# Kernel tuning notes

Measured on AMD Instinct MI355X. Metric: run time of the kernel, lower is better.

Reference implementation:

```python
import jax, jax.numpy as jnp
import numpy as np

N_EXPERTS = 8
TOP_K = 2
D_MODEL = 1024
D_FF = 4 * D_MODEL

def setup_inputs() -> dict:
    key = jax.random.key(0)
    ks = jax.random.split(key, 5)
    s_in = 1.0 / np.sqrt(D_MODEL)
    s_ff = 1.0 / np.sqrt(D_FF)
    return {
        "x": jax.random.normal(ks[0], (2, 2048, D_MODEL), dtype=jnp.float32),
        "Wr": jax.random.normal(ks[1], (N_EXPERTS, D_MODEL), dtype=jnp.float32) * s_in,
        "W1": jax.random.normal(ks[2], (N_EXPERTS, D_FF, D_MODEL), dtype=jnp.float32) * s_in,
        "W2": jax.random.normal(ks[3], (N_EXPERTS, D_MODEL, D_FF), dtype=jnp.float32) * s_ff,
        "W3": jax.random.normal(ks[4], (N_EXPERTS, D_FF, D_MODEL), dtype=jnp.float32) * s_in,
    }

def reference(x, Wr, W1, W2, W3):
    B, S, D = x.shape
    T = B * S
    xf = x.reshape(T, D)
    logits = xf @ Wr.T                         # [T, E]
    probs = jax.nn.softmax(logits, axis=-1)
    top_p, top_i = jax.lax.top_k(probs, TOP_K)  # [T, K]
    top_p = top_p / jnp.sum(top_p, axis=-1, keepdims=True)
    # per-token combine weight for each expert: [T, E]
    onehot = jax.nn.one_hot(top_i, N_EXPERTS, dtype=x.dtype)  # [T, K, E]
    cw = jnp.einsum('tke,tk->te', onehot, top_p)
    out = jnp.zeros_like(xf)
    for e in range(N_EXPERTS):  # fixed small structural loop over experts
        h = jax.nn.silu(xf @ W1[e].T) * (xf @ W3[e].T)  # [T, F]
        y = h @ W2[e].T                                 # [T, D]
        out = out + cw[:, e:e+1] * y
    importance = jnp.sum(probs, axis=0)                 # [E]
    load = jnp.sum(jnp.sum(onehot, axis=1), axis=0)     # [E]
    aux_loss = jnp.sum(importance * load) * (N_EXPERTS / (T ** 2 + 1e-06))
    return out.reshape(B, S, D), aux_loss
```

## Files before the change

### kernel.cpp

```cpp
#include <hip/hip_runtime.h>

#define T_TOK 4096
#define DM 1024
#define DF 4096
#define NE 8
#define BM 256
#define RCAP 10240
#define MAXT 40
#define ACH_B 32768
#define CHUNK_B 8192

typedef _Float16 f16x8 __attribute__((ext_vector_type(8)));
typedef float f32x4 __attribute__((ext_vector_type(4)));

#define MFMA16(a, b, c) __builtin_amdgcn_mfma_f32_16x16x32_f16(a, b, c, 0, 0, 0)
#define RAW_BAR() __builtin_amdgcn_s_barrier()
#define VMCNT(n) asm volatile("s_waitcnt vmcnt(" #n ")" ::: "memory")

__device__ __forceinline__ ushort f2h_bits(float f) {
    _Float16 h = (_Float16)f;
    return __builtin_bit_cast(unsigned short, h);
}

__device__ __forceinline__ unsigned int pk2(float a, float b) {
    return __builtin_bit_cast(unsigned int, __builtin_amdgcn_cvt_pkrtz(a, b));
}

__device__ __forceinline__ uint4 pack8(float4 a, float4 b) {
    uint4 r;
    r.x = pk2(a.x, a.y); r.y = pk2(a.z, a.w);
    r.z = pk2(b.x, b.y); r.w = pk2(b.z, b.w);
    return r;
}

__device__ __forceinline__ void gll16(const void* g, void* l) {
    __builtin_amdgcn_global_load_lds(
        (const __attribute__((address_space(1))) unsigned int*)g,
        (__attribute__((address_space(3))) unsigned int*)l, 16, 0, 0);
}

__global__ __launch_bounds__(256) void k_init(float* __restrict__ out,
                                              int* __restrict__ misc,
                                              int* __restrict__ row_tok) {
    int i = blockIdx.x * 256 + threadIdx.x;
    if (i < T_TOK * DM + 1) out[i] = 0.f;
    if (i < RCAP) row_tok[i] = -1;
    if (i < 256) misc[i] = 0;
}

__global__ __launch_bounds__(64) void k_router(const float* __restrict__ x,
                                               const float* __restrict__ Wr,
                                               float* __restrict__ probs,
                                               int* __restrict__ topi,
                                               float* __restrict__ topw,
                                               int* __restrict__ cnt) {
    int t = blockIdx.x;
    int lane = threadIdx.x;
    const float* xr = x + (size_t)t * DM;
    float s[NE];
#pragma unroll
    for (int e = 0; e < NE; e++) s[e] = 0.f;
    for (int j = lane; j < DM; j += 64) {
        float xv = xr[j];
#pragma unroll
        for (int e = 0; e < NE; e++) s[e] += xv * Wr[e * DM + j];
    }
#pragma unroll
    for (int off = 32; off > 0; off >>= 1) {
#pragma unroll
        for (int e = 0; e < NE; e++) s[e] += __shfl_xor(s[e], off, 64);
    }
    if (lane == 0) {
        float mx = s[0];
#pragma unroll
        for (int e = 1; e < NE; e++) mx = fmaxf(mx, s[e]);
        float ex[NE], sum = 0.f;
#pragma unroll
        for (int e = 0; e < NE; e++) { ex[e] = expf(s[e] - mx); sum += ex[e]; }
        float inv = 1.f / sum;
        float p[NE];
#pragma unroll
        for (int e = 0; e < NE; e++) { p[e] = ex[e] * inv; probs[t * NE + e] = p[e]; }
        int i0 = 0;
#pragma unroll
        for (int e = 1; e < NE; e++) if (p[e] > p[i0]) i0 = e;
        int i1 = (i0 == 0) ? 1 : 0;
#pragma unroll
        for (int e = 0; e < NE; e++) if (e != i0 && p[e] > p[i1]) i1 = e;
        float w0 = p[i0], w1 = p[i1], winv = 1.f / (w0 + w1);
        topi[2 * t] = i0;     topw[2 * t] = w0 * winv;
        topi[2 * t + 1] = i1; topw[2 * t + 1] = w1 * winv;
        atomicAdd(&cnt[i0], 1);
        atomicAdd(&cnt[i1], 1);
    }
}

__global__ __launch_bounds__(256) void k_scan(const float* __restrict__ probs,
                                              const int* __restrict__ cnt,
                                              int* __restrict__ poff,
                                              int* __restrict__ texp,
                                              float* __restrict__ aux_out) {
    __shared__ float red[256 * NE];
    int tid = threadIdx.x;
    float part[NE];
#pragma unroll
    for (int e = 0; e < NE; e++) part[e] = 0.f;
    for (int t = tid; t < T_TOK; t += 256) {
#pragma unroll
        for (int e = 0; e < NE; e++) part[e] += probs[t * NE + e];
    }
#pragma unroll
    for (int e = 0; e < NE; e++) red[tid * NE + e] = part[e];
    __syncthreads();
    for (int s2 = 128; s2 > 0; s2 >>= 1) {
        if (tid < s2) {
#pragma unroll
            for (int e = 0; e < NE; e++) red[tid * NE + e] += red[(tid + s2) * NE + e];
        }
        __syncthreads();
    }
    if (tid == 0) {
        float al = 0.f;
#pragma unroll
        for (int e = 0; e < NE; e++) al += red[e] * (float)cnt[e];
        *aux_out = al * (8.0f / (16777216.0f + 1e-6f));
        int run = 0, tix = 0;
        for (int e = 0; e < NE; e++) {
            poff[e] = run;
            int nt = (cnt[e] + BM - 1) / BM;
            for (int i = 0; i < nt; i++) texp[tix++] = e;
            run += nt * BM;
        }
    }
}

__global__ __launch_bounds__(256) void k_assign(const int* __restrict__ topi,
                                                const float* __restrict__ topw,
                                                const int* __restrict__ poff,
                                                int* __restrict__ fill,
                                                int* __restrict__ row_tok,
                                                float* __restrict__ row_w) {
    int t = blockIdx.x * 256 + threadIdx.x;
    if (t >= T_TOK) return;
#pragma unroll
    for (int k = 0; k < 2; k++) {
        int e = topi[2 * t + k];
        int pos = atomicAdd(&fill[e], 1);
        int r = poff[e] + pos;
        row_tok[r] = t;
        row_w[r] = topw[2 * t + k];
    }
}

__global__ __launch_bounds__(256) void k_convert(const float* __restrict__ src,
                                                 ushort* __restrict__ dst,
                                                 int row_len) {
    int nk = row_len >> 6;
    int kt = blockIdx.x, rt = blockIdx.y;
    int tid = threadIdx.x;
    int r = tid >> 2, c0 = (tid & 3) * 16;
    const float* s = src + (size_t)(rt * 64 + r) * row_len + kt * 64 + c0;
    float4 v0 = *(const float4*)(s);
    float4 v1 = *(const float4*)(s + 4);
    float4 v2 = *(const float4*)(s + 8);
    float4 v3 = *(const float4*)(s + 12);
    char* chunk = (char*)dst + ((size_t)rt * nk + kt) * CHUNK_B;
    int sw = (r & 7) << 4;
    *(uint4*)(chunk + r * 128 + ((2 * c0) ^ sw)) = pack8(v0, v1);
    *(uint4*)(chunk + r * 128 + ((2 * c0 + 16) ^ sw)) = pack8(v2, v3);
}

__global__ __launch_bounds__(512) void k_gather_t(const float* __restrict__ x,
                                                  const int* __restrict__ row_tok,
                                                  ushort* __restrict__ xg) {
    int kt = blockIdx.x, rt = blockIdx.y;
    int tid = threadIdx.x;
    int r = tid >> 1, c0 = (tid & 1) * 32;
    int tok = row_tok[rt * BM + r];
    char* chunk = (char*)xg + ((size_t)rt * 16 + kt) * ACH_B;
    int sw = (r & 7) << 4;
    if (tok >= 0) {
        const float* s = x + (size_t)tok * DM + kt * 64 + c0;
#pragma unroll
        for (int j = 0; j < 4; j++) {
            float4 va = *(const float4*)(s + j * 8);
            float4 vb = *(const float4*)(s + j * 8 + 4);
            *(uint4*)(chunk + r * 128 + ((c0 * 2 + j * 16) ^ sw)) = pack8(va, vb);
        }
    } else {
        uint4 z = {0, 0, 0, 0};
#pragma unroll
        for (int j = 0; j < 4; j++)
            *(uint4*)(chunk + r * 128 + ((c0 * 2 + j * 16) ^ sw)) = z;
    }
}

__global__ __launch_bounds__(512, 2) void k_g1(const ushort* __restrict__ xg,
                                               const ushort* __restrict__ W1h,
                                               const ushort* __restrict__ W3h,
                                               const int* __restrict__ texp,
                                               ushort* __restrict__ hbuf) {
    __shared__ __align__(16) char lds[131072];
    int b = blockIdx.x;
    int sz = (b & 7) * 160 + (b >> 3);
    int ct = sz / MAXT, rt = sz % MAXT;
    int e = texp[rt];
    int tid = threadIdx.x, lane = tid & 63, wv = tid >> 6;
    int wr = wv >> 1, wc = wv & 1;

    const char* Ac  = (const char*)xg + (size_t)rt * 16 * ACH_B;
    const char* B1c = (const char*)W1h + ((size_t)(e * 64 + ct * 2) * 16) * CHUNK_B;
    const char* B3c = (const char*)W3h + ((size_t)(e * 64 + ct * 2) * 16) * CHUNK_B;

    const f32x4 fz = {0.f, 0.f, 0.f, 0.f};
    f32x4 acc1[4][4], acc3[4][4];
#pragma unroll
    for (int m = 0; m < 4; m++)
#pragma unroll
        for (int n = 0; n < 4; n++) { acc1[m][n] = fz; acc3[m][n] = fz; }

    f16x8 af[4], bf[4];
    int kb_base = (lane >> 4) * 16;

#define ST_A(kt_, b_, h_) {                                                        \
        const char* s_ = Ac + (kt_) * ACH_B + (h_) * 16384 + wv * 2048 + lane * 16; \
        char* d_ = lds + (b_) * 65536 + (h_) * 16384 + wv * 2048;                   \
        gll16(s_, d_); gll16(s_ + 1024, d_ + 1024); }
#define ST_B(Bc_, kt_, b_, off_) {                                                          \
        gll16(Bc_ + (kt_) * 8192 + wv * 1024 + lane * 16,                                    \
              lds + (b_) * 65536 + (off_) + wv * 1024);                                      \
        gll16(Bc_ + 131072 + (kt_) * 8192 + wv * 1024 + lane * 16,                           \
              lds + (b_) * 65536 + (off_) + 8192 + wv * 1024); }
#define DS_A(b_, ks_) _Pragma("unroll") for (int m = 0; m < 4; m++) {              \
        int r_ = wr * 64 + m * 16 + (lane & 15);                                   \
        af[m] = *(const f16x8*)(lds + (b_) * 65536 + r_ * 128 +                    \
                                 (((ks_) * 64 + kb_base) ^ ((r_ & 7) << 4))); }
#define DS_B(b_, off_, ks_) _Pragma("unroll") for (int n = 0; n < 4; n++) {        \
        int c_ = wc * 64 + n * 16 + (lane & 15);                                   \
        bf[n] = *(const f16x8*)(lds + (b_) * 65536 + (off_) + c_ * 128 +           \
                                 (((ks_) * 64 + kb_base) ^ ((c_ & 7) << 4))); }
#define MM(accX) _Pragma("unroll") for (int n = 0; n < 4; n++)                     \
        _Pragma("unroll") for (int m = 0; m < 4; m++)                              \
            accX[m][n] = MFMA16(af[m], bf[n], accX[m][n]);

    ST_A(0, 0, 0); ST_A(0, 0, 1); ST_B(B1c, 0, 0, 32768); ST_B(B3c, 0, 0, 49152);
    VMCNT(2);
    RAW_BAR();

    for (int it = 0; it < 8; ++it) {
        int t1 = 2 * it + 1;
        int t2 = 2 * it + 2;
        DS_A(0, 0); DS_B(0, 32768, 0);
        ST_A(t1, 1, 0);
        RAW_BAR();
        __builtin_amdgcn_s_setprio(1); MM(acc1); __builtin_amdgcn_s_setprio(0);
        VMCNT(2);
        RAW_BAR();
        DS_B(0, 49152, 0);
        ST_A(t1, 1, 1);
        RAW_BAR();
        __builtin_amdgcn_s_setprio(1); MM(acc3); __builtin_amdgcn_s_setprio(0);
        RAW_BAR();
        DS_A(0, 1); DS_B(0, 32768, 1);
        ST_B(B1c, t1, 1, 32768);
        RAW_BAR();
        __builtin_amdgcn_s_setprio(1); MM(acc1); __builtin_amdgcn_s_setprio(0);
        RAW_BAR();
        DS_B(0, 49152, 1);
        ST_B(B3c, t1, 1, 49152);
        RAW_BAR();
        __builtin_amdgcn_s_setprio(1); MM(acc3); __builtin_amdgcn_s_setprio(0);
        VMCNT(2);
        RAW_BAR();
        DS_A(1, 0); DS_B(1, 32768, 0);
        if (it < 7) ST_A(t2, 0, 0);
        RAW_BAR();
        __builtin_amdgcn_s_setprio(1); MM(acc1); __builtin_amdgcn_s_setprio(0);
        if (it < 7) { VMCNT(2); } else { VMCNT(0); }
        RAW_BAR();
        DS_B(1, 49152, 0);
        if (it < 7) ST_A(t2, 0, 1);
        RAW_BAR();
        __builtin_amdgcn_s_setprio(1); MM(acc3); __builtin_amdgcn_s_setprio(0);
        RAW_BAR();
        DS_A(1, 1); DS_B(1, 32768, 1);
        if (it < 7) ST_B(B1c, t2, 0, 32768);
        RAW_BAR();
        __builtin_amdgcn_s_setprio(1); MM(acc1); __builtin_amdgcn_s_setprio(0);
        RAW_BAR();
        DS_B(1, 49152, 1);
        if (it < 7) ST_B(B3c, t2, 0, 49152);
        RAW_BAR();
        __builtin_amdgcn_s_setprio(1); MM(acc3); __builtin_amdgcn_s_setprio(0);
        if (it < 7) { VMCNT(2); }
        RAW_BAR();
    }
#undef ST_A
#undef ST_B
#undef DS_A
#undef DS_B
#undef MM

#pragma unroll
    for (int m = 0; m < 4; m++) {
#pragma unroll
        for (int i = 0; i < 4; i++) {
            int rl = wr * 64 + m * 16 + (lane >> 4) * 4 + i;
            int sw = (rl & 7) << 4;
#pragma unroll
            for (int n = 0; n < 4; n++) {
                int fl = wc * 64 + n * 16 + (lane & 15);
                float a1 = acc1[m][n][i], a3 = acc3[m][n][i];
                float h = (a1 / (1.f + expf(-a1))) * a3;
                char* hc = (char*)hbuf + ((size_t)rt * 64 + ct * 2 + (fl >> 6)) * ACH_B;
                *(ushort*)(hc + rl * 128 + ((2 * (fl & 63)) ^ sw)) = f2h_bits(h);
            }
        }
    }
}

__global__ __launch_bounds__(512, 1) void k_g2(const ushort* __restrict__ hbuf,
                                               const ushort* __restrict__ W2h,
                                               const int* __restrict__ texp,
                                               const int* __restrict__ row_tok,
                                               const float* __restrict__ row_w,
                                               float* __restrict__ out) {
    __shared__ __align__(16) char lds[147456];
    int b = blockIdx.x;
    int sz = (b & 7) * MAXT + (b >> 3);
    int ct = sz / MAXT, rt = sz % MAXT;
    int e = texp[rt];
    int tid = threadIdx.x, lane = tid & 63, wv = tid >> 6;
    int wr = wv >> 1, wc = wv & 1;

    const char* Ac = (const char*)hbuf + (size_t)rt * 64 * ACH_B;
    const char* Bc = (const char*)W2h + ((size_t)(e * 16 + ct * 2) * 64) * CHUNK_B;

    const f32x4 fz = {0.f, 0.f, 0.f, 0.f};
    f32x4 acc[4][4];
#pragma unroll
    for (int m = 0; m < 4; m++)
#pragma unroll
        for (int n = 0; n < 4; n++) acc[m][n] = fz;

    f16x8 af[4], bf[4];
    int kb_base = (lane >> 4) * 16;

#define BUF3(t_) (((t_) % 3) * 49152)
#define ST2_A(kt_) {                                                                 \
        const char* s_ = Ac + (size_t)(kt_) * ACH_B + wv * 4096 + lane * 16;         \
        char* d_ = lds + BUF3(kt_) + wv * 4096;                                      \
        gll16(s_, d_); gll16(s_ + 1024, d_ + 1024);                                  \
        gll16(s_ + 2048, d_ + 2048); gll16(s_ + 3072, d_ + 3072); }
#define ST2_B(kt_) {                                                                 \
        gll16(Bc + (size_t)(kt_) * 8192 + wv * 1024 + lane * 16,                     \
              lds + BUF3(kt_) + 32768 + wv * 1024);                                  \
        gll16(Bc + 524288 + (size_t)(kt_) * 8192 + wv * 1024 + lane * 16,            \
              lds + BUF3(kt_) + 40960 + wv * 1024); }
#define DS2_A(bo_, ks_) _Pragma("unroll") for (int m = 0; m < 4; m++) {              \
        int r_ = wr * 64 + m * 16 + (lane & 15);                                     \
        af[m] = *(const f16x8*)(lds + (bo_) + r_ * 128 +                             \
                                 (((ks_) * 64 + kb_base) ^ ((r_ & 7) << 4))); }
#define DS2_B(bo_, ks_) _Pragma("unroll") for (int n = 0; n < 4; n++) {              \
        int c_ = wc * 64 + n * 16 + (lane & 15);                                     \
        bf[n] = *(const f16x8*)(lds + (bo_) + 32768 + c_ * 128 +                     \
                                 (((ks_) * 64 + kb_base) ^ ((c_ & 7) << 4))); }
#define MM2() _Pragma("unroll") for (int n = 0; n < 4; n++)                          \
        _Pragma("unroll") for (int m = 0; m < 4; m++)                                \
            acc[m][n] = MFMA16(af[m], bf[n], acc[m][n]);

    ST2_A(0); ST2_B(0);
    ST2_A(1); ST2_B(1);
    VMCNT(6);
    RAW_BAR();

    for (int t = 0; t < 64; ++t) {
        int bo = BUF3(t);
        DS2_A(bo, 0); DS2_B(bo, 0);
        if (t < 62) ST2_A(t + 2);
        RAW_BAR();
        __builtin_amdgcn_s_setprio(1); MM2(); __builtin_amdgcn_s_setprio(0);
        RAW_BAR();
        DS2_A(bo, 1); DS2_B(bo, 1);
        if (t < 62) ST2_B(t + 2);
        RAW_BAR();
        __builtin_amdgcn_s_setprio(1); MM2(); __builtin_amdgcn_s_setprio(0);
        if (t < 62) { VMCNT(6); }
        else if (t == 62) { VMCNT(0); }
        RAW_BAR();
    }
#undef BUF3
#undef ST2_A
#undef ST2_B
#undef DS2_A
#undef DS2_B
#undef MM2

#pragma unroll
    for (int m = 0; m < 4; m++) {
#pragma unroll
        for (int i = 0; i < 4; i++) {
            int rr = rt * BM + wr * 64 + m * 16 + (lane >> 4) * 4 + i;
            int tok = row_tok[rr];
            if (tok >= 0) {
                float w = row_w[rr];
                float* orow = out + (size_t)tok * DM + ct * 128 + wc * 64 + (lane & 15);
#pragma unroll
                for (int n = 0; n < 4; n++) atomicAdd(&orow[n * 16], w * acc[m][n][i]);
            }
        }
    }
}

extern "C" void kernel_launch(void* const* d_in, const int* in_sizes, int n_in,
                              void* d_out, int out_size, void* d_ws, size_t ws_size,
                              hipStream_t stream) {
    (void)in_sizes; (void)n_in; (void)out_size; (void)ws_size;
    const float* x  = (const float*)d_in[0];
    const float* Wr = (const float*)d_in[1];
    const float* W1 = (const float*)d_in[2];
    const float* W2 = (const float*)d_in[3];
    const float* W3 = (const float*)d_in[4];
    float* out = (float*)d_out;
    char* ws = (char*)d_ws;

    int* misc  = (int*)ws;
    int* cnt   = misc;
    int* fill  = misc + 8;
    int* poff  = misc + 16;
    int* texp  = misc + 24;
    int*    topi    = (int*)(ws + 1024);
    float*  topw    = (float*)(ws + 33792);
    float*  probs   = (float*)(ws + 66560);
    int*    row_tok = (int*)(ws + 197632);
    float*  row_w   = (float*)(ws + 238592);
    ushort* hbuf    = (ushort*)(ws + 279552);
    ushort* W1h     = (ushort*)(ws + 84165632);
    ushort* W3h     = (ushort*)(ws + 151274496);
    ushort* xg      = (ushort*)(ws + 218383360);
    ushort* W2h     = (ushort*)(ws + 218383360);

    k_init<<<(T_TOK * DM + 1 + 255) / 256, 256, 0, stream>>>(out, misc, row_tok);
    k_router<<<T_TOK, 64, 0, stream>>>(x, Wr, probs, topi, topw, cnt);
    k_scan<<<1, 256, 0, stream>>>(probs, cnt, poff, texp, out + (size_t)T_TOK * DM);
    k_assign<<<(T_TOK + 255) / 256, 256, 0, stream>>>(topi, topw, poff, fill, row_tok, row_w);

    k_convert<<<dim3(16, 512), 256, 0, stream>>>(W1, W1h, DM);
    k_convert<<<dim3(16, 512), 256, 0, stream>>>(W3, W3h, DM);
    k_gather_t<<<dim3(16, MAXT), 512, 0, stream>>>(x, row_tok, xg);
    k_g1<<<32 * MAXT, 512, 0, stream>>>(xg, W1h, W3h, texp, hbuf);
    k_convert<<<dim3(64, 128), 256, 0, stream>>>(W2, W2h, DF);
    k_g2<<<8 * MAXT, 512, 0, stream>>>(hbuf, W2h, texp, row_tok, row_w, out);
}
```

Before: 637.1 us.

## Shrink down-projection tiles to 128x64 and early-exit unused row tiles

The second expert GEMM now uses 128-row by 64-column tiles with 256 threads and half the LDS, launched as 1280 blocks instead of 320. This gives more parallelism and two blocks per CU. Both GEMM kernels now return early for row tiles beyond the real padded token count, which is computed in the scan kernel along with a finer tile-to-expert map. Smaller tiles lower per-block data reuse and add more atomic traffic per output. A pack helper is also renamed.

```diff
diff --git a/kernel.cpp b/kernel.cpp
--- a/kernel.cpp
+++ b/kernel.cpp
@@ -7,6 +7,7 @@
 #define BM 256
 #define RCAP 10240
 #define MAXT 40
+#define MAXT2 80
 #define ACH_B 32768
 #define CHUNK_B 8192
 
@@ -26,7 +27,7 @@
     return __builtin_bit_cast(unsigned int, __builtin_amdgcn_cvt_pkrtz(a, b));
 }
 
-__device__ __forceinline__ uint4 pack8(float4 a, float4 b) {
+__device__ __forceinline__ uint4 pack8f(float4 a, float4 b) {
     uint4 r;
     r.x = pk2(a.x, a.y); r.y = pk2(a.z, a.w);
     r.z = pk2(b.x, b.y); r.w = pk2(b.z, b.w);
@@ -99,6 +100,8 @@
                                               const int* __restrict__ cnt,
                                               int* __restrict__ poff,
                                               int* __restrict__ texp,
+                                              int* __restrict__ texp2,
+                                              int* __restrict__ ntp,
                                               float* __restrict__ aux_out) {
     __shared__ float red[256 * NE];
     int tid = threadIdx.x;
@@ -131,6 +134,9 @@
             for (int i = 0; i < nt; i++) texp[tix++] = e;
             run += nt * BM;
         }
+        ntp[0] = run / BM;
+        ntp[1] = run / 128;
+        for (int j = 0; j < MAXT2; j++) texp2[j] = (j >> 1) < tix ? texp[j >> 1] : 0;
     }
 }
 
@@ -166,8 +172,8 @@
     float4 v3 = *(const float4*)(s + 12);
     char* chunk = (char*)dst + ((size_t)rt * nk + kt) * CHUNK_B;
     int sw = (r & 7) << 4;
-    *(uint4*)(chunk + r * 128 + ((2 * c0) ^ sw)) = pack8(v0, v1);
-    *(uint4*)(chunk + r * 128 + ((2 * c0 + 16) ^ sw)) = pack8(v2, v3);
+    *(uint4*)(chunk + r * 128 + ((2 * c0) ^ sw)) = pack8f(v0, v1);
+    *(uint4*)(chunk + r * 128 + ((2 * c0 + 16) ^ sw)) = pack8f(v2, v3);
 }
 
 __global__ __launch_bounds__(512) void k_gather_t(const float* __restrict__ x,
@@ -185,7 +191,7 @@
         for (int j = 0; j < 4; j++) {
             float4 va = *(const float4*)(s + j * 8);
             float4 vb = *(const float4*)(s + j * 8 + 4);
-            *(uint4*)(chunk + r * 128 + ((c0 * 2 + j * 16) ^ sw)) = pack8(va, vb);
+            *(uint4*)(chunk + r * 128 + ((c0 * 2 + j * 16) ^ sw)) = pack8f(va, vb);
         }
     } else {
         uint4 z = {0, 0, 0, 0};
@@ -199,11 +205,13 @@
                                                const ushort* __restrict__ W1h,
                                                const ushort* __restrict__ W3h,
                                                const int* __restrict__ texp,
+                                               const int* __restrict__ ntp,
                                                ushort* __restrict__ hbuf) {
     __shared__ __align__(16) char lds[131072];
     int b = blockIdx.x;
     int sz = (b & 7) * 160 + (b >> 3);
     int ct = sz / MAXT, rt = sz % MAXT;
+    if (rt >= ntp[0]) return;
     int e = texp[rt];
     int tid = threadIdx.x, lane = tid & 63, wv = tid >> 6;
     int wr = wv >> 1, wc = wv & 1;
@@ -319,53 +327,54 @@
     }
 }
 
-__global__ __launch_bounds__(512, 1) void k_g2(const ushort* __restrict__ hbuf,
+__global__ __launch_bounds__(256, 2) void k_g2(const ushort* __restrict__ hbuf,
                                                const ushort* __restrict__ W2h,
-                                               const int* __restrict__ texp,
+                                               const int* __restrict__ texp2,
+                                               const int* __restrict__ ntp,
                                                const int* __restrict__ row_tok,
                                                const float* __restrict__ row_w,
                                                float* __restrict__ out) {
-    __shared__ __align__(16) char lds[147456];
+    __shared__ __align__(16) char lds[73728];
     int b = blockIdx.x;
-    int sz = (b & 7) * MAXT + (b >> 3);
-    int ct = sz / MAXT, rt = sz % MAXT;
-    int e = texp[rt];
+    int sz = (b & 7) * 160 + (b >> 3);
+    int ct = sz / MAXT2, rt2 = sz % MAXT2;
+    if (rt2 >= ntp[1]) return;
+    int e = texp2[rt2];
     int tid = threadIdx.x, lane = tid & 63, wv = tid >> 6;
     int wr = wv >> 1, wc = wv & 1;
 
-    const char* Ac = (const char*)hbuf + (size_t)rt * 64 * ACH_B;
-    const char* Bc = (const char*)W2h + ((size_t)(e * 16 + ct * 2) * 64) * CHUNK_B;
+    const char* Ac = (const char*)hbuf + ((size_t)(rt2 >> 1) * 64) * ACH_B + (rt2 & 1) * 16384;
+    const char* Bc = (const char*)W2h + ((size_t)(e * 16 + ct) * 64) * CHUNK_B;
 
     const f32x4 fz = {0.f, 0.f, 0.f, 0.f};
-    f32x4 acc[4][4];
+    f32x4 acc[4][2];
 #pragma unroll
     for (int m = 0; m < 4; m++)
 #pragma unroll
-        for (int n = 0; n < 4; n++) acc[m][n] = fz;
-
-    f16x8 af[4], bf[4];
+        for (int n = 0; n < 2; n++) acc[m][n] = fz;
+
+    f16x8 af[4], bf[2];
     int kb_base = (lane >> 4) * 16;
 
-#define BUF3(t_) (((t_) % 3) * 49152)
+#define BUF3(t_) (((t_) % 3) * 24576)
 #define ST2_A(kt_) {                                                                 \
         const char* s_ = Ac + (size_t)(kt_) * ACH_B + wv * 4096 + lane * 16;         \
         char* d_ = lds + BUF3(kt_) + wv * 4096;                                      \
         gll16(s_, d_); gll16(s_ + 1024, d_ + 1024);                                  \
         gll16(s_ + 2048, d_ + 2048); gll16(s_ + 3072, d_ + 3072); }
 #define ST2_B(kt_) {                                                                 \
-        gll16(Bc + (size_t)(kt_) * 8192 + wv * 1024 + lane * 16,                     \
-              lds + BUF3(kt_) + 32768 + wv * 1024);                                  \
-        gll16(Bc + 524288 + (size_t)(kt_) * 8192 + wv * 1024 + lane * 16,            \
-              lds + BUF3(kt_) + 40960 + wv * 1024); }
+        const char* s_ = Bc + (size_t)(kt_) * 8192 + wv * 2048 + lane * 16;          \
+        char* d_ = lds + BUF3(kt_) + 16384 + wv * 2048;                              \
+        gll16(s_, d_); gll16(s_ + 1024, d_ + 1024); }
 #define DS2_A(bo_, ks_) _Pragma("unroll") for (int m = 0; m < 4; m++) {              \
         int r_ = wr * 64 + m * 16 + (lane & 15);                                     \
         af[m] = *(const f16x8*)(lds + (bo_) + r_ * 128 +                             \
                                  (((ks_) * 64 + kb_base) ^ ((r_ & 7) << 4))); }
-#define DS2_B(bo_, ks_) _Pragma("unroll") for (int n = 0; n < 4; n++) {              \
-        int c_ = wc * 64 + n * 16 + (lane & 15);                                     \
-        bf[n] = *(const f16x8*)(lds + (bo_) + 32768 + c_ * 128 +                     \
+#define DS2_B(bo_, ks_) _Pragma("unroll") for (int n = 0; n < 2; n++) {              \
+        int c_ = wc * 32 + n * 16 + (lane & 15);                                     \
+        bf[n] = *(const f16x8*)(lds + (bo_) + 16384 + c_ * 128 +                     \
                                  (((ks_) * 64 + kb_base) ^ ((c_ & 7) << 4))); }
-#define MM2() _Pragma("unroll") for (int n = 0; n < 4; n++)                          \
+#define MM2() _Pragma("unroll") for (int n = 0; n < 2; n++)                          \
         _Pragma("unroll") for (int m = 0; m < 4; m++)                                \
             acc[m][n] = MFMA16(af[m], bf[n], acc[m][n]);
 
@@ -400,13 +409,13 @@
     for (int m = 0; m < 4; m++) {
 #pragma unroll
         for (int i = 0; i < 4; i++) {
-            int rr = rt * BM + wr * 64 + m * 16 + (lane >> 4) * 4 + i;
+            int rr = rt2 * 128 + wr * 64 + m * 16 + (lane >> 4) * 4 + i;
             int tok = row_tok[rr];
             if (tok >= 0) {
                 float w = row_w[rr];
-                float* orow = out + (size_t)tok * DM + ct * 128 + wc * 64 + (lane & 15);
-#pragma unroll
-                for (int n = 0; n < 4; n++) atomicAdd(&orow[n * 16], w * acc[m][n][i]);
+                float* orow = out + (size_t)tok * DM + ct * 64 + wc * 32 + (lane & 15);
+#pragma unroll
+                for (int n = 0; n < 2; n++) atomicAdd(&orow[n * 16], w * acc[m][n][i]);
             }
         }
     }
@@ -429,6 +438,8 @@
     int* fill  = misc + 8;
     int* poff  = misc + 16;
     int* texp  = misc + 24;
+    int* texp2 = misc + 64;
+    int* ntp   = misc + 144;
     int*    topi    = (int*)(ws + 1024);
     float*  topw    = (float*)(ws + 33792);
     float*  probs   = (float*)(ws + 66560);
@@ -442,13 +453,13 @@
 
     k_init<<<(T_TOK * DM + 1 + 255) / 256, 256, 0, stream>>>(out, misc, row_tok);
     k_router<<<T_TOK, 64, 0, stream>>>(x, Wr, probs, topi, topw, cnt);
-    k_scan<<<1, 256, 0, stream>>>(probs, cnt, poff, texp, out + (size_t)T_TOK * DM);
+    k_scan<<<1, 256, 0, stream>>>(probs, cnt, poff, texp, texp2, ntp, out + (size_t)T_TOK * DM);
     k_assign<<<(T_TOK + 255) / 256, 256, 0, stream>>>(topi, topw, poff, fill, row_tok, row_w);
 
     k_convert<<<dim3(16, 512), 256, 0, stream>>>(W1, W1h, DM);
     k_convert<<<dim3(16, 512), 256, 0, stream>>>(W3, W3h, DM);
     k_gather_t<<<dim3(16, MAXT), 512, 0, stream>>>(x, row_tok, xg);
-    k_g1<<<32 * MAXT, 512, 0, stream>>>(xg, W1h, W3h, texp, hbuf);
+    k_g1<<<32 * MAXT, 512, 0, stream>>>(xg, W1h, W3h, texp, ntp, hbuf);
     k_convert<<<dim3(64, 128), 256, 0, stream>>>(W2, W2h, DF);
-    k_g2<<<8 * MAXT, 512, 0, stream>>>(hbuf, W2h, texp, row_tok, row_w, out);
-}
+    k_g2<<<8 * MAXT2 * 2, 256, 0, stream>>>(hbuf, W2h, texp2, ntp, row_tok, row_w, out);
+}
```

After: 677.9 us. 1.06x slower.
